# Performance work log

Hardware: AMD Instinct MI355X
Metric: run time of the kernel (lower is better)

The kernel has to match this reference:

```python
import jax, jax.numpy as jnp
import numpy as np

VOCAB = 32000


def setup_inputs() -> dict:
    key = jax.random.key(0)
    ks = jax.random.split(key, 8)
    B, T, S, H = 8, 256, 400, 512
    return {
        "s_output": jax.random.normal(ks[0], (B, T, H), jnp.float32),
        "state_input": jax.random.normal(ks[1], (B, T, 2 * H), jnp.float32),
        "attn_scores": jax.random.uniform(ks[2], (B, T, S), jnp.float32),
        "enc_batch_extend_vocab": jax.random.randint(ks[3], (B, S), 0, VOCAB),
        "w_pgen": jax.random.normal(ks[4], (2 * H, 1), jnp.float32) * 0.02,
        "b_pgen": jnp.zeros((1,), jnp.float32),
        "w1": jax.random.normal(ks[5], (H, H), jnp.float32) * 0.02,
        "b1": jnp.zeros((H,), jnp.float32),
        "w2": jax.random.normal(ks[6], (H, VOCAB), jnp.float32) * 0.02,
        "b2": jnp.zeros((VOCAB,), jnp.float32),
    }


def reference(s_output, state_input, attn_scores, enc_batch_extend_vocab,
              w_pgen, b_pgen, w1, b1, w2, b2):
    B, T, S = attn_scores.shape
    # generation gate: sigmoid(Linear(state_input))  -> [B, T, 1]
    p_gen = jax.nn.sigmoid(state_input @ w_pgen + b_pgen)
    # vocab distribution: softmax(Linear(Linear(s_output)))  -> [B, T, V]
    logits = (s_output @ w1 + b1) @ w2 + b2
    vocab_dist = jax.nn.softmax(logits, axis=-1)
    vocab_dist_ = p_gen * vocab_dist              # [B, T, V]
    attn_dist_ = (1.0 - p_gen) * attn_scores      # [B, T, S]
    # scatter_add attention mass into vocab positions (collisions accumulate)
    bi = jnp.arange(B)[:, None, None]
    ti = jnp.arange(T)[None, :, None]
    si = enc_batch_extend_vocab[:, None, :]       # [B, 1, S] broadcasts to [B, T, S]
    final_dist = vocab_dist_.at[bi, ti, si].add(attn_dist_) + 1e-12
    return jnp.log(final_dist).reshape(-1, final_dist.shape[-1])
```

## Files before the change

### kernel.cpp

```cpp
#include <hip/hip_runtime.h>
#include <hip/hip_bf16.h>
#include <stdint.h>

#define BB 8
#define TT 256
#define SS 400
#define HH 512
#define VV 32000
#define MM (BB*TT)
#define KK 512

#define BM2 256
#define BN2 256
#define BK2 64
#define NBLK2 (VV/BN2)
#define MBLK2 (MM/BM2)
#define G2B (NBLK2*MBLK2)

typedef __bf16 bf16x8 __attribute__((ext_vector_type(8)));
typedef float  f32x4  __attribute__((ext_vector_type(4)));
typedef unsigned short ushort8 __attribute__((ext_vector_type(8)));

__device__ __forceinline__ unsigned short f2bf(float x) {
    union { float f; unsigned u; } v; v.f = x;
    unsigned r = v.u + 0x7fffu + ((v.u >> 16) & 1u);
    return (unsigned short)(r >> 16);
}
__device__ __forceinline__ float bf2f(unsigned short u) {
    union { unsigned u; float f; } v; v.u = ((unsigned)u) << 16; return v.f;
}

__device__ __forceinline__ void async_ld16(const void* g, void* lds) {
    __builtin_amdgcn_global_load_lds(
        (const __attribute__((address_space(1))) unsigned int*)g,
        (__attribute__((address_space(3))) unsigned int*)lds,
        16, 0, 0);
}

__global__ __launch_bounds__(256) void f32_to_bf16_kernel(const float* __restrict__ x,
                                                          unsigned short* __restrict__ y, int n4) {
    int i = blockIdx.x * blockDim.x + threadIdx.x;
    if (i < n4) {
        float4 v = ((const float4*)x)[i];
        ushort4 o;
        o.x = f2bf(v.x); o.y = f2bf(v.y); o.z = f2bf(v.z); o.w = f2bf(v.w);
        ((ushort4*)y)[i] = o;
    }
}

__global__ __launch_bounds__(256) void transpose_bf16_kernel(const float* __restrict__ W,
                                                             unsigned short* __restrict__ Wt,
                                                             int K, int N) {
    __shared__ float tile[32][33];
    int n0 = blockIdx.x * 32, k0 = blockIdx.y * 32;
    int t = threadIdx.x;
    int r  = t >> 3;
    int c4 = (t & 7) * 4;
    float4 v = *(const float4*)(W + (size_t)(k0 + r) * N + n0 + c4);
    tile[r][c4 + 0] = v.x; tile[r][c4 + 1] = v.y;
    tile[r][c4 + 2] = v.z; tile[r][c4 + 3] = v.w;
    __syncthreads();
    ushort4 o;
    o.x = f2bf(tile[c4 + 0][r]);
    o.y = f2bf(tile[c4 + 1][r]);
    o.z = f2bf(tile[c4 + 2][r]);
    o.w = f2bf(tile[c4 + 3][r]);
    *(ushort4*)(Wt + (size_t)(n0 + r) * K + k0 + c4) = o;
}

__global__ __launch_bounds__(256) void pgen_kernel(const float* __restrict__ state,
                                                   const float* __restrict__ wp,
                                                   const float* __restrict__ bp,
                                                   float* __restrict__ pg) {
    int row  = blockIdx.x * 4 + (threadIdx.x >> 6);
    int lane = threadIdx.x & 63;
    const float* s = state + (size_t)row * (2 * HH);
    float acc = 0.f;
    for (int j = lane; j < 2 * HH; j += 64) acc += s[j] * wp[j];
    for (int off = 32; off; off >>= 1) acc += __shfl_xor(acc, off, 64);
    if (lane == 0) pg[row] = 1.f / (1.f + __expf(-(acc + bp[0])));
}

__global__ __launch_bounds__(256) void gemm1_kernel(const unsigned short* __restrict__ A,
                                                    const unsigned short* __restrict__ Bt,
                                                    const float* __restrict__ bias,
                                                    unsigned short* __restrict__ out, int N) {
    __shared__ __align__(16) unsigned short As[128 * 32];
    __shared__ __align__(16) unsigned short Bs[128 * 32];
    const int tid = threadIdx.x, wave = tid >> 6, lane = tid & 63;
    const int m0 = blockIdx.y * 128, n0 = blockIdx.x * 128;
    const int q = lane >> 4, r_ = lane & 15;
    const int wm = (wave >> 1) * 64, wn = (wave & 1) * 64;
    f32x4 acc[4][4] = {};
    for (int k0 = 0; k0 < KK; k0 += 32) {
        #pragma unroll
        for (int rr = 0; rr < 2; ++rr) {
            int cc = tid + rr * 256, row = cc >> 2, col = (cc & 3) * 8;
            async_ld16(A  + (size_t)(m0 + row) * KK + k0 + col, (char*)As + (size_t)cc * 16);
            async_ld16(Bt + (size_t)(n0 + row) * KK + k0 + col, (char*)Bs + (size_t)cc * 16);
        }
        __syncthreads();
        bf16x8 a[4], b[4];
        #pragma unroll
        for (int i = 0; i < 4; ++i) {
            a[i] = *(const bf16x8*)(As + (wm + i * 16 + r_) * 32 + q * 8);
            b[i] = *(const bf16x8*)(Bs + (wn + i * 16 + r_) * 32 + q * 8);
        }
        #pragma unroll
        for (int mi = 0; mi < 4; ++mi)
            #pragma unroll
            for (int ni = 0; ni < 4; ++ni)
                acc[mi][ni] = __builtin_amdgcn_mfma_f32_16x16x32_bf16(a[mi], b[ni], acc[mi][ni], 0, 0, 0);
        __syncthreads();
    }
    #pragma unroll
    for (int mi = 0; mi < 4; ++mi)
        #pragma unroll
        for (int ni = 0; ni < 4; ++ni) {
            int n = n0 + wn + ni * 16 + r_;
            float bv = bias[n];
            #pragma unroll
            for (int rg = 0; rg < 4; ++rg) {
                int m = m0 + wm + mi * 16 + q * 4 + rg;
                out[(size_t)m * N + n] = f2bf(acc[mi][ni][rg] + bv);
            }
        }
}

template <bool E_BF16>
__global__ __launch_bounds__(512, 2) void gemm2_exp_kernel(const unsigned short* __restrict__ A,
                                                           const unsigned short* __restrict__ Bt,
                                                           const float* __restrict__ bias,
                                                           void* __restrict__ E,
                                                           float* __restrict__ Zpart) {
    __shared__ __align__(16) char lds[2][65536];
    const int tid = threadIdx.x, wave = tid >> 6, lane = tid & 63;
    const int q = lane >> 4, r_ = lane & 15;
    const int wm = wave >> 2;
    const int wn = wave & 3;

    const int bid = blockIdx.x;
    const int xcd = bid & 7;
    const int sub = bid >> 3;
    const int lin = xcd * (G2B / 8) + sub;
    const int nb  = lin >> 3;
    const int mb  = lin & 7;
    const int m0 = mb * BM2, n0 = nb * BN2;

    f32x4 acc[8][4] = {};

    auto stage = [&](int t, int j) {
        int c   = tid + j * 512;
        int row = c >> 3;
        int colb = (c & 7) * 16;
        int src  = colb ^ ((row & 7) << 4);
        char* base = lds[t & 1];
        async_ld16((const char*)A  + ((size_t)(m0 + row) * KK + t * BK2) * 2 + src,
                   base + c * 16);
        async_ld16((const char*)Bt + ((size_t)(n0 + row) * KK + t * BK2) * 2 + src,
                   base + 32768 + c * 16);
    };

    #pragma unroll
    for (int j = 0; j < 4; ++j) stage(0, j);
    asm volatile("s_waitcnt vmcnt(0)" ::: "memory");
    __builtin_amdgcn_s_barrier();
    __builtin_amdgcn_sched_barrier(0);

    for (int t = 0; t < KK / BK2; ++t) {
        char* buf = lds[t & 1];
        #pragma unroll
        for (int p = 0; p < 4; ++p) {
            if (t < KK / BK2 - 1) stage(t + 1, p);
            const int mib = (p >> 1) * 4;
            const int nib = (p & 1) * 2;
            bf16x8 af[4][2], bg[2][2];
            #pragma unroll
            for (int mi = 0; mi < 4; ++mi)
                #pragma unroll
                for (int ks = 0; ks < 2; ++ks) {
                    int row = wm * 128 + (mib + mi) * 16 + r_;
                    int cb  = (ks * 64 + q * 16) ^ ((row & 7) << 4);
                    af[mi][ks] = *(const bf16x8*)(buf + row * 128 + cb);
                }
            #pragma unroll
            for (int ni = 0; ni < 2; ++ni)
                #pragma unroll
                for (int ks = 0; ks < 2; ++ks) {
                    int row = wn * 64 + (nib + ni) * 16 + r_;
                    int cb  = (ks * 64 + q * 16) ^ ((row & 7) << 4);
                    bg[ni][ks] = *(const bf16x8*)(buf + 32768 + row * 128 + cb);
                }
            __builtin_amdgcn_s_setprio(1);
            #pragma unroll
            for (int mi = 0; mi < 4; ++mi)
                #pragma unroll
                for (int ni = 0; ni < 2; ++ni)
                    #pragma unroll
                    for (int ks = 0; ks < 2; ++ks)
                        acc[mib + mi][nib + ni] = __builtin_amdgcn_mfma_f32_16x16x32_bf16(
                            af[mi][ks], bg[ni][ks], acc[mib + mi][nib + ni], 0, 0, 0);
            __builtin_amdgcn_s_setprio(0);
            __builtin_amdgcn_sched_barrier(0);
            __builtin_amdgcn_s_barrier();
            __builtin_amdgcn_sched_barrier(0);
        }
        asm volatile("s_waitcnt vmcnt(0)" ::: "memory");
        __builtin_amdgcn_sched_barrier(0);
        __builtin_amdgcn_s_barrier();
        __builtin_amdgcn_sched_barrier(0);
    }

    float* rowsum = (float*)&lds[0][0];
    if (tid < BM2) rowsum[tid] = 0.f;
    __syncthreads();

    float bv[4];
    #pragma unroll
    for (int ni = 0; ni < 4; ++ni) bv[ni] = bias[n0 + wn * 64 + ni * 16 + r_];

    #pragma unroll
    for (int mi = 0; mi < 8; ++mi) {
        float rp[4] = {0.f, 0.f, 0.f, 0.f};
        #pragma unroll
        for (int ni = 0; ni < 4; ++ni) {
            int n = n0 + wn * 64 + ni * 16 + r_;
            #pragma unroll
            for (int rg = 0; rg < 4; ++rg) {
                int m = m0 + wm * 128 + mi * 16 + q * 4 + rg;
                float e = __expf(acc[mi][ni][rg] + bv[ni]);
                if (E_BF16)
                    ((unsigned short*)E)[(size_t)m * VV + n] = f2bf(e);
                else
                    ((float*)E)[(size_t)m * VV + n] = e;
                rp[rg] += e;
            }
        }
        #pragma unroll
        for (int rg = 0; rg < 4; ++rg) {
            float v = rp[rg];
            v += __shfl_xor(v, 1, 64);
            v += __shfl_xor(v, 2, 64);
            v += __shfl_xor(v, 4, 64);
            v += __shfl_xor(v, 8, 64);
            if (r_ == 0) atomicAdd(&rowsum[wm * 128 + mi * 16 + q * 4 + rg], v);
        }
    }
    __syncthreads();
    if (tid < BM2) Zpart[(size_t)nb * MM + m0 + tid] = rowsum[tid];
}

__global__ __launch_bounds__(256) void zfinal_kernel(const float* __restrict__ Zpart,
                                                     float* __restrict__ Z) {
    int row = blockIdx.x * 256 + threadIdx.x;
    float s = 0.f;
    for (int nb = 0; nb < NBLK2; ++nb) s += Zpart[(size_t)nb * MM + row];
    Z[row] = s;
}

template <bool E_BF16>
__global__ __launch_bounds__(256) void finalize_kernel(const void* __restrict__ E,
                                                       float* __restrict__ out,
                                                       const float* __restrict__ pg_arr,
                                                       const float* __restrict__ Z,
                                                       const float* __restrict__ attn,
                                                       const int* __restrict__ enc) {
    constexpr int CH = VV / 8;
    __shared__ float acc[CH];
    int bid = blockIdx.x;
    int row = bid >> 3;
    int part = bid & 7;
    int nbase = part * CH;
    f32x4* acc4 = (f32x4*)acc;
    for (int j = threadIdx.x; j < CH / 4; j += 256) acc4[j] = (f32x4){0.f, 0.f, 0.f, 0.f};
    float pg = pg_arr[row];
    float scale = pg / Z[row];
    float om = 1.f - pg;
    int batch = row / TT;
    __syncthreads();
    for (int s = threadIdx.x; s < SS; s += 256) {
        int idx = enc[batch * SS + s];
        if (idx >= nbase && idx < nbase + CH)
            atomicAdd(&acc[idx - nbase], om * attn[(size_t)row * SS + s]);
    }
    __syncthreads();
    size_t base = (size_t)row * VV + nbase;
    for (int j = threadIdx.x * 8; j < CH; j += 2048) {
        float e[8];
        if (E_BF16) {
            ushort8 u = *(const ushort8*)((const unsigned short*)E + base + j);
            #pragma unroll
            for (int i = 0; i < 8; ++i) e[i] = bf2f(u[i]);
        } else {
            f32x4 u0 = *(const f32x4*)((const float*)E + base + j);
            f32x4 u1 = *(const f32x4*)((const float*)E + base + j + 4);
            e[0]=u0[0]; e[1]=u0[1]; e[2]=u0[2]; e[3]=u0[3];
            e[4]=u1[0]; e[5]=u1[1]; e[6]=u1[2]; e[7]=u1[3];
        }
        f32x4 a0 = acc4[(j >> 2) + 0];
        f32x4 a1 = acc4[(j >> 2) + 1];
        f32x4 o0, o1;
        #pragma unroll
        for (int i = 0; i < 4; ++i) o0[i] = __logf(scale * e[i]     + a0[i] + 1e-12f);
        #pragma unroll
        for (int i = 0; i < 4; ++i) o1[i] = __logf(scale * e[4 + i] + a1[i] + 1e-12f);
        *(f32x4*)(out + base + j)     = o0;
        *(f32x4*)(out + base + j + 4) = o1;
    }
}

extern "C" void kernel_launch(void* const* d_in, const int* in_sizes, int n_in,
                              void* d_out, int out_size, void* d_ws, size_t ws_size,
                              hipStream_t stream) {
    const float* s_output = (const float*)d_in[0];
    const float* state_in = (const float*)d_in[1];
    const float* attn     = (const float*)d_in[2];
    const int*   enc      = (const int*)  d_in[3];
    const float* w_pgen   = (const float*)d_in[4];
    const float* b_pgen   = (const float*)d_in[5];
    const float* w1       = (const float*)d_in[6];
    const float* b1       = (const float*)d_in[7];
    const float* w2       = (const float*)d_in[8];
    const float* b2       = (const float*)d_in[9];

    char* ws = (char*)d_ws;
    float*          pg     = (float*)(ws + 0);
    float*          Z      = (float*)(ws + 8192);
    unsigned short* hidden = (unsigned short*)(ws + 16384);
    unsigned short* sA     = (unsigned short*)(ws + 2113536);
    float*          Zpart  = (float*)(ws + 2113536);
    unsigned short* w1t    = (unsigned short*)(ws + 4210688);
    unsigned short* w2t    = (unsigned short*)(ws + 4734976);
    unsigned short* Ebf    = (unsigned short*)(ws + 37502976);

    const size_t NEED_BIG = 37502976ull + 2ull * MM * VV;
    const bool big = (ws_size >= NEED_BIG);

    f32_to_bf16_kernel<<<(MM * HH / 4 + 255) / 256, 256, 0, stream>>>(s_output, sA, MM * HH / 4);
    transpose_bf16_kernel<<<dim3(HH / 32, KK / 32), 256, 0, stream>>>(w1, w1t, KK, HH);
    transpose_bf16_kernel<<<dim3(VV / 32, KK / 32), 256, 0, stream>>>(w2, w2t, KK, VV);
    pgen_kernel<<<MM / 4, 256, 0, stream>>>(state_in, w_pgen, b_pgen, pg);
    gemm1_kernel<<<dim3(HH / 128, MM / 128), 256, 0, stream>>>(sA, w1t, b1, hidden, HH);

    if (big) {
        gemm2_exp_kernel<true><<<G2B, 512, 0, stream>>>(hidden, w2t, b2, Ebf, Zpart);
        zfinal_kernel<<<MM / 256, 256, 0, stream>>>(Zpart, Z);
        finalize_kernel<true><<<MM * 8, 256, 0, stream>>>(Ebf, (float*)d_out, pg, Z, attn, enc);
    } else {
        gemm2_exp_kernel<false><<<G2B, 512, 0, stream>>>(hidden, w2t, b2, d_out, Zpart);
        zfinal_kernel<<<MM / 256, 256, 0, stream>>>(Zpart, Z);
        finalize_kernel<false><<<MM * 8, 256, 0, stream>>>(d_out, (float*)d_out, pg, Z, attn, enc);
    }
}
```

Before: 511.5 us.

## Use triple-buffered BK=32 LDS pipeline in vocab GEMM with one barrier per step

Replaces the double-buffered 64-wide K tile, which had four sub-phases and a barrier after each, with a three-stage ring of 32-wide K tiles. Loads run two stages ahead and are gated by a partial vmcnt wait, leaving a single barrier per K step. The LDS swizzle is changed to fit the 64-byte rows. This aims to cut barrier overhead and expose more load/compute overlap, at the cost of smaller tiles per step and more loop iterations.

```diff
diff --git a/kernel.cpp b/kernel.cpp
--- a/kernel.cpp
+++ b/kernel.cpp
@@ -12,7 +12,8 @@
 
 #define BM2 256
 #define BN2 256
-#define BK2 64
+#define BK2 32
+#define NT2 (KK/BK2)
 #define NBLK2 (VV/BN2)
 #define MBLK2 (MM/BM2)
 #define G2B (NBLK2*MBLK2)
@@ -133,7 +134,7 @@
                                                            const float* __restrict__ bias,
                                                            void* __restrict__ E,
                                                            float* __restrict__ Zpart) {
-    __shared__ __align__(16) char lds[2][65536];
+    __shared__ __align__(16) char lds[3][32768];
     const int tid = threadIdx.x, wave = tid >> 6, lane = tid & 63;
     const int q = lane >> 4, r_ = lane & 15;
     const int wm = wave >> 2;
@@ -149,68 +150,59 @@
 
     f32x4 acc[8][4] = {};
 
-    auto stage = [&](int t, int j) {
-        int c   = tid + j * 512;
-        int row = c >> 3;
-        int colb = (c & 7) * 16;
-        int src  = colb ^ ((row & 7) << 4);
-        char* base = lds[t & 1];
-        async_ld16((const char*)A  + ((size_t)(m0 + row) * KK + t * BK2) * 2 + src,
-                   base + c * 16);
-        async_ld16((const char*)Bt + ((size_t)(n0 + row) * KK + t * BK2) * 2 + src,
-                   base + 32768 + c * 16);
+    auto stage = [&](int t) {
+        char* base = lds[t % 3];
+        #pragma unroll
+        for (int j = 0; j < 2; ++j) {
+            int c    = tid + j * 512;
+            int row  = c >> 2;
+            int colb = (c & 3) * 16;
+            int swz  = (((row & 3) ^ ((row >> 2) & 3)) << 4);
+            int src  = colb ^ swz;
+            async_ld16((const char*)A  + ((size_t)(m0 + row) * KK + t * BK2) * 2 + src,
+                       base + c * 16);
+            async_ld16((const char*)Bt + ((size_t)(n0 + row) * KK + t * BK2) * 2 + src,
+                       base + 16384 + c * 16);
+        }
     };
 
-    #pragma unroll
-    for (int j = 0; j < 4; ++j) stage(0, j);
-    asm volatile("s_waitcnt vmcnt(0)" ::: "memory");
-    __builtin_amdgcn_s_barrier();
-    __builtin_amdgcn_sched_barrier(0);
-
-    for (int t = 0; t < KK / BK2; ++t) {
-        char* buf = lds[t & 1];
-        #pragma unroll
-        for (int p = 0; p < 4; ++p) {
-            if (t < KK / BK2 - 1) stage(t + 1, p);
-            const int mib = (p >> 1) * 4;
-            const int nib = (p & 1) * 2;
-            bf16x8 af[4][2], bg[2][2];
-            #pragma unroll
-            for (int mi = 0; mi < 4; ++mi)
-                #pragma unroll
-                for (int ks = 0; ks < 2; ++ks) {
-                    int row = wm * 128 + (mib + mi) * 16 + r_;
-                    int cb  = (ks * 64 + q * 16) ^ ((row & 7) << 4);
-                    af[mi][ks] = *(const bf16x8*)(buf + row * 128 + cb);
-                }
-            #pragma unroll
-            for (int ni = 0; ni < 2; ++ni)
-                #pragma unroll
-                for (int ks = 0; ks < 2; ++ks) {
-                    int row = wn * 64 + (nib + ni) * 16 + r_;
-                    int cb  = (ks * 64 + q * 16) ^ ((row & 7) << 4);
-                    bg[ni][ks] = *(const bf16x8*)(buf + 32768 + row * 128 + cb);
-                }
-            __builtin_amdgcn_s_setprio(1);
-            #pragma unroll
-            for (int mi = 0; mi < 4; ++mi)
-                #pragma unroll
-                for (int ni = 0; ni < 2; ++ni)
-                    #pragma unroll
-                    for (int ks = 0; ks < 2; ++ks)
-                        acc[mib + mi][nib + ni] = __builtin_amdgcn_mfma_f32_16x16x32_bf16(
-                            af[mi][ks], bg[ni][ks], acc[mib + mi][nib + ni], 0, 0, 0);
-            __builtin_amdgcn_s_setprio(0);
-            __builtin_amdgcn_sched_barrier(0);
-            __builtin_amdgcn_s_barrier();
-            __builtin_amdgcn_sched_barrier(0);
-        }
-        asm volatile("s_waitcnt vmcnt(0)" ::: "memory");
+    stage(0);
+    stage(1);
+
+    for (int t = 0; t < NT2; ++t) {
+        if (t < NT2 - 1) asm volatile("s_waitcnt vmcnt(4)" ::: "memory");
+        else             asm volatile("s_waitcnt vmcnt(0)" ::: "memory");
         __builtin_amdgcn_sched_barrier(0);
         __builtin_amdgcn_s_barrier();
         __builtin_amdgcn_sched_barrier(0);
-    }
-
+        if (t + 2 < NT2) stage(t + 2);
+
+        char* buf = lds[t % 3];
+        bf16x8 af[8], bg[4];
+        #pragma unroll
+        for (int mi = 0; mi < 8; ++mi) {
+            int row = wm * 128 + mi * 16 + r_;
+            int cb  = (q * 16) ^ (((row & 3) ^ ((row >> 2) & 3)) << 4);
+            af[mi] = *(const bf16x8*)(buf + row * 64 + cb);
+        }
+        #pragma unroll
+        for (int ni = 0; ni < 4; ++ni) {
+            int row = wn * 64 + ni * 16 + r_;
+            int cb  = (q * 16) ^ (((row & 3) ^ ((row >> 2) & 3)) << 4);
+            bg[ni] = *(const bf16x8*)(buf + 16384 + row * 64 + cb);
+        }
+        __builtin_amdgcn_s_setprio(1);
+        #pragma unroll
+        for (int mi = 0; mi < 8; ++mi)
+            #pragma unroll
+            for (int ni = 0; ni < 4; ++ni)
+                acc[mi][ni] = __builtin_amdgcn_mfma_f32_16x16x32_bf16(
+                    af[mi], bg[ni], acc[mi][ni], 0, 0, 0);
+        __builtin_amdgcn_s_setprio(0);
+        __builtin_amdgcn_sched_barrier(0);
+    }
+
+    __syncthreads();
     float* rowsum = (float*)&lds[0][0];
     if (tid < BM2) rowsum[tid] = 0.f;
     __syncthreads();
```

Result: no change. 510.9 us (-0.1%).
